# Kernel optimization log

Measured on AMD Instinct MI355X. Metric: run time of the kernel, lower is better.

## Reference

```python
import jax, jax.numpy as jnp
import numpy as np

EMBED_DIM = 1024
NUM_HEADS = 16
B, L = 4, 2048


def setup_inputs() -> dict:
    key = jax.random.key(0)
    ks = jax.random.split(key, 5)
    scale = 0.02
    return {
        "x": jax.random.normal(ks[0], (B, L, EMBED_DIM), dtype=jnp.float32),
        "Wqkv_w": jax.random.normal(ks[1], (3 * EMBED_DIM, EMBED_DIM), dtype=jnp.float32) * scale,
        "Wqkv_b": jax.random.normal(ks[2], (3 * EMBED_DIM,), dtype=jnp.float32) * scale,
        "out_w": jax.random.normal(ks[3], (EMBED_DIM, EMBED_DIM), dtype=jnp.float32) * scale,
        "out_b": jax.random.normal(ks[4], (EMBED_DIM,), dtype=jnp.float32) * scale,
    }


def reference(x, Wqkv_w, Wqkv_b, out_w, out_b):
    Bb, Ll, D = x.shape
    H = NUM_HEADS
    hd = D // H
    # fused QKV projection (torch Linear: x @ W.T + b)
    qkv = jnp.einsum("bld,ed->ble", x, Wqkv_w) + Wqkv_b  # [B, L, 3D]
    q, k, v = jnp.split(qkv, 3, axis=-1)
    # [B, H, L, hd]
    q = q.reshape(Bb, Ll, H, hd).transpose(0, 2, 1, 3)
    k = k.reshape(Bb, Ll, H, hd).transpose(0, 2, 1, 3)
    v = v.reshape(Bb, Ll, H, hd).transpose(0, 2, 1, 3)
    scale = 1.0 / jnp.sqrt(jnp.asarray(hd, dtype=x.dtype))
    scores = jnp.einsum("bhqd,bhkd->bhqk", q, k) * scale  # [B, H, L, L]
    # causal mask (upper triangle above diagonal masked)
    causal = jnp.tril(jnp.ones((Ll, Ll), dtype=bool))
    scores = jnp.where(causal, scores, jnp.asarray(-jnp.inf, dtype=scores.dtype))
    attn = jax.nn.softmax(scores, axis=-1)
    attn_out = jnp.einsum("bhqk,bhkd->bhqd", attn, v)  # [B, H, L, hd]
    attn_out = attn_out.transpose(0, 2, 1, 3).reshape(Bb, Ll, D)
    out = jnp.einsum("bld,ed->ble", attn_out, out_w) + out_b
    return out
```

## Files before the change

### kernel.cpp

```cpp
#include <hip/hip_runtime.h>
#include <stdint.h>

#define DEV __device__ __forceinline__

typedef unsigned short u16;
typedef __bf16 bf16x8 __attribute__((ext_vector_type(8)));
typedef float f32x4 __attribute__((ext_vector_type(4)));
typedef u16 u16x8 __attribute__((ext_vector_type(8)));

#define MFMA_BF16(A, B, C) __builtin_amdgcn_mfma_f32_16x16x32_bf16(A, B, C, 0, 0, 0)
#define EXP2(x) __builtin_amdgcn_exp2f(x)

DEV u16 f2bf(float f) {
    unsigned x;
    __builtin_memcpy(&x, &f, 4);
    unsigned r = (x + 0x7fffu + ((x >> 16) & 1u)) >> 16;
    return (u16)r;
}

DEV u16 f2bf_fast(float f) {
    unsigned x;
    __builtin_memcpy(&x, &f, 4);
    return (u16)((x + 0x8000u) >> 16);
}

DEV void storeC(u16* p, float v) { *p = f2bf(v); }
DEV void storeC(float* p, float v) { *p = v; }

DEV void async_copy16(const u16* g, u16* l) {
    __builtin_amdgcn_global_load_lds(
        (__attribute__((address_space(1))) unsigned int*)g,
        (__attribute__((address_space(3))) unsigned int*)l, 16, 0, 0);
}

DEV void wg_barrier() {
    asm volatile("" ::: "memory");
    __builtin_amdgcn_s_barrier();
    asm volatile("" ::: "memory");
}

constexpr int N_X = 8192 * 1024, N_WQ = 3072 * 1024, N_WO = 1024 * 1024;

__global__ __launch_bounds__(256)
void cvt_all(const float* __restrict__ x, const float* __restrict__ wq,
             const float* __restrict__ wo, u16* __restrict__ out) {
    const int i = (blockIdx.x * 256 + threadIdx.x) * 4;
    const float* src;
    if (i < N_X) src = x + i;
    else if (i < N_X + N_WQ) src = wq + (i - N_X);
    else src = wo + (i - N_X - N_WQ);
    const float4 v = *(const float4*)src;
    ushort4 o;
    o.x = f2bf(v.x);
    o.y = f2bf(v.y);
    o.z = f2bf(v.z);
    o.w = f2bf(v.w);
    *(ushort4*)(out + i) = o;
}

template <typename OT, bool VSPLIT>
__global__ __launch_bounds__(512, 2)
void gemm_8ph(const u16* __restrict__ A, const u16* __restrict__ Bw,
              const float* __restrict__ bias, OT* __restrict__ C,
              u16* __restrict__ vT, int M, int N, int K, int ntn) {
    __shared__ __attribute__((aligned(16))) u16 sA[3][256 * 64];
    __shared__ __attribute__((aligned(16))) u16 sB[3][128 * 64];

    const int tid  = threadIdx.x;
    const int lane = tid & 63;
    const int wave = tid >> 6;
    const int fr = lane & 15;
    const int q4 = lane >> 4;
    const int wr = wave >> 1;
    const int wc = wave & 1;

    const int cpx = gridDim.x >> 3;
    const int wg = (blockIdx.x & 7) * cpx + (blockIdx.x >> 3);
    const int mt = wg / ntn, nt = wg % ntn;
    const int m0 = mt * 256, n0 = nt * 128;

    const int crow = tid >> 3;
    const int ccol = ((tid & 7) ^ (crow & 7)) * 8;
    const u16* pA = A + (size_t)(m0 + crow) * K + ccol;
    const u16* pB = Bw + (size_t)(n0 + crow) * K + ccol;
    const size_t rK = (size_t)64 * K;

    const int NT = K >> 6;

    f32x4 acc[4][4];
#pragma unroll
    for (int i = 0; i < 4; i++)
#pragma unroll
        for (int j = 0; j < 4; j++) acc[i][j] = (f32x4){0.f, 0.f, 0.f, 0.f};

#pragma unroll
    for (int p = 0; p < 4; p++) async_copy16(pA + p * rK, &sA[0][p * 4096 + tid * 8]);
#pragma unroll
    for (int p = 0; p < 2; p++) async_copy16(pB + p * rK, &sB[0][p * 4096 + tid * 8]);
#pragma unroll
    for (int p = 0; p < 4; p++) async_copy16(pA + p * rK + 64, &sA[1][p * 4096 + tid * 8]);
#pragma unroll
    for (int p = 0; p < 2; p++) async_copy16(pB + p * rK + 64, &sB[1][p * 4096 + tid * 8]);
    asm volatile("s_waitcnt vmcnt(6)" ::: "memory");
    wg_barrier();

    int sl = 0;
    for (int t = 0; t < NT; ++t) {
        const u16* bufA = sA[sl];
        const u16* bufB = sB[sl];
        const int s2 = (sl >= 1) ? sl - 1 : 2;
        const bool st = (t + 2 < NT);
        const int ko = (t + 2) * 64;

        bf16x8 af[4][2], bf[4][2];

#pragma unroll
        for (int i = 0; i < 4; i++) {
            const int row = wr * 64 + i * 16 + fr;
#pragma unroll
            for (int kk = 0; kk < 2; kk++)
                af[i][kk] = *(const bf16x8*)
                    &bufA[row * 64 + (((kk * 64 + q4 * 16) ^ ((row & 7) << 4)) >> 1)];
        }
#pragma unroll
        for (int j = 0; j < 2; j++) {
            const int row = wc * 64 + j * 16 + fr;
#pragma unroll
            for (int kk = 0; kk < 2; kk++)
                bf[j][kk] = *(const bf16x8*)
                    &bufB[row * 64 + (((kk * 64 + q4 * 16) ^ ((row & 7) << 4)) >> 1)];
        }
        if (st) {
#pragma unroll
            for (int p = 0; p < 3; p++)
                async_copy16(pA + p * rK + ko, &sA[s2][p * 4096 + tid * 8]);
        }
        wg_barrier();
        __builtin_amdgcn_s_setprio(1);
#pragma unroll
        for (int i = 0; i < 4; i++)
#pragma unroll
            for (int j = 0; j < 2; j++) {
                acc[i][j] = MFMA_BF16(af[i][0], bf[j][0], acc[i][j]);
                acc[i][j] = MFMA_BF16(af[i][1], bf[j][1], acc[i][j]);
            }
        __builtin_amdgcn_s_setprio(0);
        wg_barrier();

#pragma unroll
        for (int j = 2; j < 4; j++) {
            const int row = wc * 64 + j * 16 + fr;
#pragma unroll
            for (int kk = 0; kk < 2; kk++)
                bf[j][kk] = *(const bf16x8*)
                    &bufB[row * 64 + (((kk * 64 + q4 * 16) ^ ((row & 7) << 4)) >> 1)];
        }
        if (st) {
            async_copy16(pA + 3 * rK + ko, &sA[s2][3 * 4096 + tid * 8]);
#pragma unroll
            for (int p = 0; p < 2; p++)
                async_copy16(pB + p * rK + ko, &sB[s2][p * 4096 + tid * 8]);
        }
        if (t < NT - 2) asm volatile("s_waitcnt vmcnt(6)" ::: "memory");
        else            asm volatile("s_waitcnt vmcnt(0)" ::: "memory");
        wg_barrier();
        __builtin_amdgcn_s_setprio(1);
#pragma unroll
        for (int i = 0; i < 4; i++)
#pragma unroll
            for (int j = 2; j < 4; j++) {
                acc[i][j] = MFMA_BF16(af[i][0], bf[j][0], acc[i][j]);
                acc[i][j] = MFMA_BF16(af[i][1], bf[j][1], acc[i][j]);
            }
        __builtin_amdgcn_s_setprio(0);
        wg_barrier();

        sl = (sl < 2) ? sl + 1 : 0;
    }

#pragma unroll
    for (int j = 0; j < 4; j++) {
        const int col = n0 + wc * 64 + j * 16 + fr;
        const float bv = bias[col];
        if (VSPLIT && col >= 2048) {
#pragma unroll
            for (int i = 0; i < 4; i++) {
                const int row = m0 + wr * 64 + i * 16 + q4 * 4;
                ushort4 o;
                o.x = f2bf(acc[i][j][0] + bv);
                o.y = f2bf(acc[i][j][1] + bv);
                o.z = f2bf(acc[i][j][2] + bv);
                o.w = f2bf(acc[i][j][3] + bv);
                *(ushort4*)&vT[(size_t)(col - 2048) * 8192 + row] = o;
            }
        } else {
#pragma unroll
            for (int i = 0; i < 4; i++) {
                const int row = m0 + wr * 64 + i * 16 + q4 * 4;
#pragma unroll
                for (int r = 0; r < 4; r++)
                    storeC(&C[(size_t)(row + r) * N + col], acc[i][j][r] + bv);
            }
        }
    }
}

constexpr int Lc = 2048, Dc = 1024;

__global__ __launch_bounds__(256, 4)
void attn_fa(const u16* __restrict__ qkv, const u16* __restrict__ vT,
             u16* __restrict__ outb) {
    __shared__ __attribute__((aligned(16))) u16 sK[64 * 72];
    __shared__ __attribute__((aligned(16))) u16 sVT[64 * 72];
    __shared__ __attribute__((aligned(16))) u16 sP[4][2][16 * 72];

    const int tid  = threadIdx.x;
    const int lane = tid & 63;
    const int wave = tid >> 6;
    const int fr = lane & 15;
    const int q4 = lane >> 4;

    const int id = blockIdx.x;
    const int g  = (id & 7) + 8 * (id >> 7);
    const int bx = (id >> 3) & 15;
    const int h = g & 15;
    const int b = g >> 4;
    const int qblkA = bx;
    const int qblkB = 31 - bx;

    constexpr float CEXP = 0.18033688011112042f;

    const int qrowA = qblkA * 64 + wave * 16 + fr;
    const int qrowB = qblkB * 64 + wave * 16 + fr;
    const u16* qptrA = qkv + ((size_t)(b * Lc + qrowA) * 3) * Dc + h * 64;
    const u16* qptrB = qkv + ((size_t)(b * Lc + qrowB) * 3) * Dc + h * 64;
    bf16x8 qfA[2], qfB[2];
    qfA[0] = *(const bf16x8*)(qptrA + q4 * 8);
    qfA[1] = *(const bf16x8*)(qptrA + 32 + q4 * 8);
    qfB[0] = *(const bf16x8*)(qptrB + q4 * 8);
    qfB[1] = *(const bf16x8*)(qptrB + 32 + q4 * 8);

    f32x4 oA[4], oB[4];
#pragma unroll
    for (int t = 0; t < 4; t++) {
        oA[t] = (f32x4){0.f, 0.f, 0.f, 0.f};
        oB[t] = (f32x4){0.f, 0.f, 0.f, 0.f};
    }
    float mA = -3.4e38f, lA = 0.f, mB = -3.4e38f, lB = 0.f;

    const int q_local = wave * 16 + fr;

    const int rr = tid >> 3;
    const int oo = tid & 7;
    const u16* kg = qkv + ((size_t)(b * Lc) * 3 + 1) * Dc + h * 64 + oo * 8;
    const u16* vg = vT + (size_t)(h * 64) * 8192 + b * Lc + oo * 8;

    u16x8 kr[2], vr[2];
#pragma unroll
    for (int c = 0; c < 2; ++c) {
        kr[c] = *(const u16x8*)(kg + (size_t)(c * 32 + rr) * 3072);
        vr[c] = *(const u16x8*)(vg + (size_t)(c * 32 + rr) * 8192);
    }

    u16* sPA = &sP[wave][0][0];
    u16* sPB = &sP[wave][1][0];

    for (int jb = 0; jb <= qblkB; ++jb) {
        __syncthreads();
#pragma unroll
        for (int c = 0; c < 2; ++c) {
            *(u16x8*)&sK[(c * 32 + rr) * 72 + oo * 8] = kr[c];
            *(u16x8*)&sVT[(c * 32 + rr) * 72 + oo * 8] = vr[c];
        }
        __syncthreads();
        if (jb < qblkB) {
#pragma unroll
            for (int c = 0; c < 2; ++c) {
                kr[c] = *(const u16x8*)(kg + (size_t)((jb + 1) * 64 + c * 32 + rr) * 3072);
                vr[c] = *(const u16x8*)(vg + (size_t)(c * 32 + rr) * 8192 + (jb + 1) * 64);
            }
        }

        const bool doA = (jb <= qblkA);

        f32x4 sA_[4], sB_[4];
#pragma unroll
        for (int t = 0; t < 4; t++) {
            const bf16x8 kf0 = *(const bf16x8*)&sK[(t * 16 + fr) * 72 + q4 * 8];
            const bf16x8 kf1 = *(const bf16x8*)&sK[(t * 16 + fr) * 72 + 32 + q4 * 8];
            sB_[t] = (f32x4){0.f, 0.f, 0.f, 0.f};
            sB_[t] = MFMA_BF16(kf0, qfB[0], sB_[t]);
            sB_[t] = MFMA_BF16(kf1, qfB[1], sB_[t]);
            if (doA) {
                sA_[t] = (f32x4){0.f, 0.f, 0.f, 0.f};
                sA_[t] = MFMA_BF16(kf0, qfA[0], sA_[t]);
                sA_[t] = MFMA_BF16(kf1, qfA[1], sA_[t]);
            }
        }

        {
            if (jb == qblkB) {
#pragma unroll
                for (int t = 0; t < 4; t++)
#pragma unroll
                    for (int r = 0; r < 4; r++)
                        if (t * 16 + q4 * 4 + r > q_local) sB_[t][r] = -1e30f;
            }
            float mx = sB_[0][0];
#pragma unroll
            for (int t = 0; t < 4; t++)
#pragma unroll
                for (int r = 0; r < 4; r++) mx = fmaxf(mx, sB_[t][r]);
            mx = fmaxf(mx, __shfl_xor(mx, 16));
            mx = fmaxf(mx, __shfl_xor(mx, 32));
            const float mnew = fmaxf(mB, mx);
            const float alpha = EXP2((mB - mnew) * CEXP);
            float sum = 0.f;
#pragma unroll
            for (int t = 0; t < 4; t++) {
#pragma unroll
                for (int r = 0; r < 4; r++) {
                    const float p = EXP2((sB_[t][r] - mnew) * CEXP);
                    sB_[t][r] = p;
                    sum += p;
                }
                ushort4 o;
                o.x = f2bf_fast(sB_[t][0]);
                o.y = f2bf_fast(sB_[t][1]);
                o.z = f2bf_fast(sB_[t][2]);
                o.w = f2bf_fast(sB_[t][3]);
                *(ushort4*)&sPB[fr * 72 + t * 16 + q4 * 4] = o;
            }
            sum += __shfl_xor(sum, 16);
            sum += __shfl_xor(sum, 32);
            lB = alpha * lB + sum;
            mB = mnew;
#pragma unroll
            for (int t = 0; t < 4; t++)
#pragma unroll
                for (int r = 0; r < 4; r++) oB[t][r] *= alpha;
        }

        if (doA) {
            if (jb == qblkA) {
#pragma unroll
                for (int t = 0; t < 4; t++)
#pragma unroll
                    for (int r = 0; r < 4; r++)
                        if (t * 16 + q4 * 4 + r > q_local) sA_[t][r] = -1e30f;
            }
            float mx = sA_[0][0];
#pragma unroll
            for (int t = 0; t < 4; t++)
#pragma unroll
                for (int r = 0; r < 4; r++) mx = fmaxf(mx, sA_[t][r]);
            mx = fmaxf(mx, __shfl_xor(mx, 16));
            mx = fmaxf(mx, __shfl_xor(mx, 32));
            const float mnew = fmaxf(mA, mx);
            const float alpha = EXP2((mA - mnew) * CEXP);
            float sum = 0.f;
#pragma unroll
            for (int t = 0; t < 4; t++) {
#pragma unroll
                for (int r = 0; r < 4; r++) {
                    const float p = EXP2((sA_[t][r] - mnew) * CEXP);
                    sA_[t][r] = p;
                    sum += p;
                }
                ushort4 o;
                o.x = f2bf_fast(sA_[t][0]);
                o.y = f2bf_fast(sA_[t][1]);
                o.z = f2bf_fast(sA_[t][2]);
                o.w = f2bf_fast(sA_[t][3]);
                *(ushort4*)&sPA[fr * 72 + t * 16 + q4 * 4] = o;
            }
            sum += __shfl_xor(sum, 16);
            sum += __shfl_xor(sum, 32);
            lA = alpha * lA + sum;
            mA = mnew;
#pragma unroll
            for (int t = 0; t < 4; t++)
#pragma unroll
                for (int r = 0; r < 4; r++) oA[t][r] *= alpha;
        }

#pragma unroll
        for (int ks = 0; ks < 2; ++ks) {
            const bf16x8 pfB = *(const bf16x8*)&sPB[fr * 72 + ks * 32 + q4 * 8];
            bf16x8 pfA;
            if (doA) pfA = *(const bf16x8*)&sPA[fr * 72 + ks * 32 + q4 * 8];
#pragma unroll
            for (int t = 0; t < 4; t++) {
                const bf16x8 vf = *(const bf16x8*)&sVT[(t * 16 + fr) * 72 + ks * 32 + q4 * 8];
                oB[t] = MFMA_BF16(vf, pfB, oB[t]);
                if (doA) oA[t] = MFMA_BF16(vf, pfA, oA[t]);
            }
        }
    }

    const float rlA = 1.0f / lA;
    const float rlB = 1.0f / lB;
    u16* orowA = outb + (size_t)(b * Lc + qblkA * 64 + wave * 16 + fr) * Dc + h * 64;
    u16* orowB = outb + (size_t)(b * Lc + qblkB * 64 + wave * 16 + fr) * Dc + h * 64;
#pragma unroll
    for (int t = 0; t < 4; t++) {
        ushort4 a, o;
        a.x = f2bf(oA[t][0] * rlA);
        a.y = f2bf(oA[t][1] * rlA);
        a.z = f2bf(oA[t][2] * rlA);
        a.w = f2bf(oA[t][3] * rlA);
        *(ushort4*)(orowA + t * 16 + q4 * 4) = a;
        o.x = f2bf(oB[t][0] * rlB);
        o.y = f2bf(oB[t][1] * rlB);
        o.z = f2bf(oB[t][2] * rlB);
        o.w = f2bf(oB[t][3] * rlB);
        *(ushort4*)(orowB + t * 16 + q4 * 4) = o;
    }
}

extern "C" void kernel_launch(void* const* d_in, const int* in_sizes, int n_in,
                              void* d_out, int out_size, void* d_ws, size_t ws_size,
                              hipStream_t stream) {
    const float* x    = (const float*)d_in[0];
    const float* wqkv = (const float*)d_in[1];
    const float* bqkv = (const float*)d_in[2];
    const float* wout = (const float*)d_in[3];
    const float* bout = (const float*)d_in[4];
    float* out = (float*)d_out;

    u16* qkv    = (u16*)d_ws;
    u16* attn   = qkv + (size_t)8192 * 3072;
    u16* xbf    = attn + (size_t)8192 * 1024;
    u16* wqkvbf = xbf + (size_t)8192 * 1024;
    u16* woutbf = wqkvbf + (size_t)3072 * 1024;
    u16* vT     = woutbf + (size_t)1024 * 1024;

    cvt_all<<<(N_X + N_WQ + N_WO) / 1024, dim3(256), 0, stream>>>(x, wqkv, wout, xbf);

    gemm_8ph<u16, true><<<dim3(768), dim3(512), 0, stream>>>(
        xbf, wqkvbf, bqkv, qkv, vT, 8192, 3072, 1024, 24);
    attn_fa<<<dim3(1024), dim3(256), 0, stream>>>(qkv, vT, attn);
    gemm_8ph<float, false><<<dim3(256), dim3(512), 0, stream>>>(
        attn, woutbf, bout, out, nullptr, 8192, 1024, 1024, 8);
}
```

Baseline: 267.9 us.

## Enlarge GEMM tiles to 256x256 with double-buffered LDS pipeline

The GEMM kernel now computes 256x256 output tiles instead of 256x128, using a 2x4 wave layout with 8x4 accumulator fragments per wave. The 3-stage LDS ring is replaced by a double buffer that prefetches the next K-slice across four MFMA phases and waits for all loads at the end of each iteration. The aim is more arithmetic per byte loaded and fewer global reads of the A operand. The trade-off is higher register and LDS use, which likely allows only one block per CU. The grid also halves, leaving the output projection with only 128 blocks.

```diff
diff --git a/kernel.cpp b/kernel.cpp
--- a/kernel.cpp
+++ b/kernel.cpp
@@ -60,123 +60,118 @@
 
 template <typename OT, bool VSPLIT>
 __global__ __launch_bounds__(512, 2)
-void gemm_8ph(const u16* __restrict__ A, const u16* __restrict__ Bw,
+void gemm_256(const u16* __restrict__ A, const u16* __restrict__ Bw,
               const float* __restrict__ bias, OT* __restrict__ C,
               u16* __restrict__ vT, int M, int N, int K, int ntn) {
-    __shared__ __attribute__((aligned(16))) u16 sA[3][256 * 64];
-    __shared__ __attribute__((aligned(16))) u16 sB[3][128 * 64];
+    __shared__ __attribute__((aligned(16))) u16 sA[2][256 * 64];
+    __shared__ __attribute__((aligned(16))) u16 sB[2][256 * 64];
 
     const int tid  = threadIdx.x;
     const int lane = tid & 63;
     const int wave = tid >> 6;
     const int fr = lane & 15;
     const int q4 = lane >> 4;
-    const int wr = wave >> 1;
-    const int wc = wave & 1;
+    const int wr = wave >> 2;
+    const int wc = wave & 3;
 
     const int cpx = gridDim.x >> 3;
     const int wg = (blockIdx.x & 7) * cpx + (blockIdx.x >> 3);
     const int mt = wg / ntn, nt = wg % ntn;
-    const int m0 = mt * 256, n0 = nt * 128;
+    const int m0 = mt * 256, n0 = nt * 256;
 
     const int crow = tid >> 3;
     const int ccol = ((tid & 7) ^ (crow & 7)) * 8;
     const u16* pA = A + (size_t)(m0 + crow) * K + ccol;
     const u16* pB = Bw + (size_t)(n0 + crow) * K + ccol;
     const size_t rK = (size_t)64 * K;
-
     const int NT = K >> 6;
 
-    f32x4 acc[4][4];
-#pragma unroll
-    for (int i = 0; i < 4; i++)
+    f32x4 acc[8][4];
+#pragma unroll
+    for (int i = 0; i < 8; i++)
 #pragma unroll
         for (int j = 0; j < 4; j++) acc[i][j] = (f32x4){0.f, 0.f, 0.f, 0.f};
 
 #pragma unroll
     for (int p = 0; p < 4; p++) async_copy16(pA + p * rK, &sA[0][p * 4096 + tid * 8]);
 #pragma unroll
-    for (int p = 0; p < 2; p++) async_copy16(pB + p * rK, &sB[0][p * 4096 + tid * 8]);
-#pragma unroll
-    for (int p = 0; p < 4; p++) async_copy16(pA + p * rK + 64, &sA[1][p * 4096 + tid * 8]);
-#pragma unroll
-    for (int p = 0; p < 2; p++) async_copy16(pB + p * rK + 64, &sB[1][p * 4096 + tid * 8]);
-    asm volatile("s_waitcnt vmcnt(6)" ::: "memory");
+    for (int p = 0; p < 4; p++) async_copy16(pB + p * rK, &sB[0][p * 4096 + tid * 8]);
+    asm volatile("s_waitcnt vmcnt(0)" ::: "memory");
     wg_barrier();
 
-    int sl = 0;
+#define RD_A(dst, rbase)                                                        \
+    _Pragma("unroll") for (int i = 0; i < 4; i++) {                             \
+        const int row_ = (rbase) + i * 16 + fr;                                 \
+        _Pragma("unroll") for (int kk = 0; kk < 2; kk++)                        \
+            dst[i][kk] = *(const bf16x8*)                                       \
+                &bufA[row_ * 64 + (((kk * 64 + q4 * 16) ^ ((row_ & 7) << 4)) >> 1)]; \
+    }
+#define RD_B(dst, rbase)                                                        \
+    _Pragma("unroll") for (int j = 0; j < 2; j++) {                             \
+        const int row_ = (rbase) + j * 16 + fr;                                 \
+        _Pragma("unroll") for (int kk = 0; kk < 2; kk++)                        \
+            dst[j][kk] = *(const bf16x8*)                                       \
+                &bufB[row_ * 64 + (((kk * 64 + q4 * 16) ^ ((row_ & 7) << 4)) >> 1)]; \
+    }
+#define PH_MFMA(mh, nh, bfv)                                                    \
+    wg_barrier();                                                               \
+    __builtin_amdgcn_s_setprio(1);                                              \
+    _Pragma("unroll") for (int i = 0; i < 4; i++)                               \
+    _Pragma("unroll") for (int j = 0; j < 2; j++) {                             \
+        acc[(mh) * 4 + i][(nh) * 2 + j] =                                       \
+            MFMA_BF16(afr[i][0], bfv[j][0], acc[(mh) * 4 + i][(nh) * 2 + j]);   \
+        acc[(mh) * 4 + i][(nh) * 2 + j] =                                       \
+            MFMA_BF16(afr[i][1], bfv[j][1], acc[(mh) * 4 + i][(nh) * 2 + j]);   \
+    }                                                                           \
+    __builtin_amdgcn_s_setprio(0);                                              \
+    wg_barrier();
+
     for (int t = 0; t < NT; ++t) {
-        const u16* bufA = sA[sl];
-        const u16* bufB = sB[sl];
-        const int s2 = (sl >= 1) ? sl - 1 : 2;
-        const bool st = (t + 2 < NT);
-        const int ko = (t + 2) * 64;
-
-        bf16x8 af[4][2], bf[4][2];
-
-#pragma unroll
-        for (int i = 0; i < 4; i++) {
-            const int row = wr * 64 + i * 16 + fr;
-#pragma unroll
-            for (int kk = 0; kk < 2; kk++)
-                af[i][kk] = *(const bf16x8*)
-                    &bufA[row * 64 + (((kk * 64 + q4 * 16) ^ ((row & 7) << 4)) >> 1)];
-        }
-#pragma unroll
-        for (int j = 0; j < 2; j++) {
-            const int row = wc * 64 + j * 16 + fr;
-#pragma unroll
-            for (int kk = 0; kk < 2; kk++)
-                bf[j][kk] = *(const bf16x8*)
-                    &bufB[row * 64 + (((kk * 64 + q4 * 16) ^ ((row & 7) << 4)) >> 1)];
-        }
+        const u16* bufA = sA[t & 1];
+        const u16* bufB = sB[t & 1];
+        u16* nxA = (u16*)sA[(t & 1) ^ 1];
+        u16* nxB = (u16*)sB[(t & 1) ^ 1];
+        const bool st = (t + 1 < NT);
+        const size_t ko = (size_t)(t + 1) * 64;
+
+        bf16x8 afr[4][2], b0[2][2], b1[2][2];
+
+        RD_A(afr, wr * 128);
+        RD_B(b0, wc * 64);
         if (st) {
 #pragma unroll
-            for (int p = 0; p < 3; p++)
-                async_copy16(pA + p * rK + ko, &sA[s2][p * 4096 + tid * 8]);
-        }
+            for (int p = 0; p < 4; p++)
+                async_copy16(pA + p * rK + ko, &nxA[p * 4096 + tid * 8]);
+        }
+        PH_MFMA(0, 0, b0);
+
+        RD_B(b1, wc * 64 + 32);
+        if (st) {
+#pragma unroll
+            for (int p = 0; p < 4; p++)
+                async_copy16(pB + p * rK + ko, &nxB[p * 4096 + tid * 8]);
+        }
+        PH_MFMA(0, 1, b1);
+
+        RD_A(afr, wr * 128 + 64);
+        PH_MFMA(1, 0, b0);
+
         wg_barrier();
         __builtin_amdgcn_s_setprio(1);
 #pragma unroll
         for (int i = 0; i < 4; i++)
 #pragma unroll
             for (int j = 0; j < 2; j++) {
-                acc[i][j] = MFMA_BF16(af[i][0], bf[j][0], acc[i][j]);
-                acc[i][j] = MFMA_BF16(af[i][1], bf[j][1], acc[i][j]);
+                acc[4 + i][2 + j] = MFMA_BF16(afr[i][0], b1[j][0], acc[4 + i][2 + j]);
+                acc[4 + i][2 + j] = MFMA_BF16(afr[i][1], b1[j][1], acc[4 + i][2 + j]);
             }
         __builtin_amdgcn_s_setprio(0);
+        asm volatile("s_waitcnt vmcnt(0)" ::: "memory");
         wg_barrier();
-
-#pragma unroll
-        for (int j = 2; j < 4; j++) {
-            const int row = wc * 64 + j * 16 + fr;
-#pragma unroll
-            for (int kk = 0; kk < 2; kk++)
-                bf[j][kk] = *(const bf16x8*)
-                    &bufB[row * 64 + (((kk * 64 + q4 * 16) ^ ((row & 7) << 4)) >> 1)];
-        }
-        if (st) {
-            async_copy16(pA + 3 * rK + ko, &sA[s2][3 * 4096 + tid * 8]);
-#pragma unroll
-            for (int p = 0; p < 2; p++)
-                async_copy16(pB + p * rK + ko, &sB[s2][p * 4096 + tid * 8]);
-        }
-        if (t < NT - 2) asm volatile("s_waitcnt vmcnt(6)" ::: "memory");
-        else            asm volatile("s_waitcnt vmcnt(0)" ::: "memory");
-        wg_barrier();
-        __builtin_amdgcn_s_setprio(1);
-#pragma unroll
-        for (int i = 0; i < 4; i++)
-#pragma unroll
-            for (int j = 2; j < 4; j++) {
-                acc[i][j] = MFMA_BF16(af[i][0], bf[j][0], acc[i][j]);
-                acc[i][j] = MFMA_BF16(af[i][1], bf[j][1], acc[i][j]);
-            }
-        __builtin_amdgcn_s_setprio(0);
-        wg_barrier();
-
-        sl = (sl < 2) ? sl + 1 : 0;
-    }
+    }
+#undef RD_A
+#undef RD_B
+#undef PH_MFMA
 
 #pragma unroll
     for (int j = 0; j < 4; j++) {
@@ -184,8 +179,8 @@
         const float bv = bias[col];
         if (VSPLIT && col >= 2048) {
 #pragma unroll
-            for (int i = 0; i < 4; i++) {
-                const int row = m0 + wr * 64 + i * 16 + q4 * 4;
+            for (int i = 0; i < 8; i++) {
+                const int row = m0 + wr * 128 + i * 16 + q4 * 4;
                 ushort4 o;
                 o.x = f2bf(acc[i][j][0] + bv);
                 o.y = f2bf(acc[i][j][1] + bv);
@@ -195,8 +190,8 @@
             }
         } else {
 #pragma unroll
-            for (int i = 0; i < 4; i++) {
-                const int row = m0 + wr * 64 + i * 16 + q4 * 4;
+            for (int i = 0; i < 8; i++) {
+                const int row = m0 + wr * 128 + i * 16 + q4 * 4;
 #pragma unroll
                 for (int r = 0; r < 4; r++)
                     storeC(&C[(size_t)(row + r) * N + col], acc[i][j][r] + bv);
@@ -437,9 +432,9 @@
 
     cvt_all<<<(N_X + N_WQ + N_WO) / 1024, dim3(256), 0, stream>>>(x, wqkv, wout, xbf);
 
-    gemm_8ph<u16, true><<<dim3(768), dim3(512), 0, stream>>>(
-        xbf, wqkvbf, bqkv, qkv, vT, 8192, 3072, 1024, 24);
+    gemm_256<u16, true><<<dim3(384), dim3(512), 0, stream>>>(
+        xbf, wqkvbf, bqkv, qkv, vT, 8192, 3072, 1024, 12);
     attn_fa<<<dim3(1024), dim3(256), 0, stream>>>(qkv, vT, attn);
-    gemm_8ph<float, false><<<dim3(256), dim3(512), 0, stream>>>(
-        attn, woutbf, bout, out, nullptr, 8192, 1024, 1024, 8);
-}
+    gemm_256<float, false><<<dim3(128), dim3(512), 0, stream>>>(
+        attn, woutbf, bout, out, nullptr, 8192, 1024, 1024, 4);
+}
```

Measured after the change: 292.5 us. 1.09x slower.
